# Optimization experiments

Measured on AMD Instinct MI355X. Metric: run time of the kernel, lower is better.

Reference implementation:

```python
import jax, jax.numpy as jnp
import numpy as np

B, T, C = 2, 2048, 1024
N_HEADS = 16
HEAD_DIM = C // N_HEADS

def setup_inputs() -> dict:
    key = jax.random.key(0)
    k1, k2, k3 = jax.random.split(key, 3)
    x = jax.random.normal(k1, (B, T, C), dtype=jnp.float32)
    W_qkv = jax.random.normal(k2, (C, 3 * C), dtype=jnp.float32) * (1.0 / np.sqrt(C))
    W_out = jax.random.normal(k3, (C, C), dtype=jnp.float32) * (1.0 / np.sqrt(C))
    return {"x": x, "W_qkv": W_qkv, "W_out": W_out}

def reference(x, W_qkv, W_out):
    b, t, c = x.shape
    qkv = jnp.einsum('btc,cd->btd', x, W_qkv)  # [B,T,3C]
    q, k, v = jnp.split(qkv, 3, axis=-1)
    # [B, H, T, hd]
    q = q.reshape(b, t, N_HEADS, HEAD_DIM).transpose(0, 2, 1, 3)
    k = k.reshape(b, t, N_HEADS, HEAD_DIM).transpose(0, 2, 1, 3)
    v = v.reshape(b, t, N_HEADS, HEAD_DIM).transpose(0, 2, 1, 3)
    scale = 1.0 / jnp.sqrt(jnp.asarray(HEAD_DIM, dtype=x.dtype))
    attn = jnp.einsum('bhqd,bhkd->bhqk', q, k) * scale  # [B,H,T,T]
    causal = jnp.tril(jnp.ones((t, t), dtype=bool))
    attn = jnp.where(causal, attn, jnp.asarray(-1e9, dtype=attn.dtype))
    attn = jax.nn.softmax(attn, axis=-1)
    out = jnp.einsum('bhqk,bhkd->bhqd', attn, v)
    out = out.transpose(0, 2, 1, 3).reshape(b, t, c)
    return jnp.einsum('btc,cd->btd', out, W_out)
```

## Files before the change

### kernel.cpp

```cpp
#include <hip/hip_runtime.h>
#include <hip/hip_bf16.h>

typedef __attribute__((ext_vector_type(8))) short short8;
typedef __attribute__((ext_vector_type(4))) short bf16x4;
typedef __attribute__((ext_vector_type(4))) float floatx4;

#define T_SEQ 2048
#define NH    16
#define HD    64
#define QSCALE 0.18033688f

#define MFMA16(a, b, c) __builtin_amdgcn_mfma_f32_16x16x16bf16_1k(a, b, c, 0, 0, 0)
#define MFMA32(a, b, c) __builtin_amdgcn_mfma_f32_16x16x32_bf16(a, b, c, 0, 0, 0)

__device__ __forceinline__ ushort f2bf(float f) {
    union { float f; unsigned u; } un; un.f = f;
    unsigned r = un.u + 0x7fff + ((un.u >> 16) & 1);
    return (ushort)(r >> 16);
}
__device__ __forceinline__ unsigned pkbf(float a, float b) {
    __hip_bfloat162 t = __float22bfloat162_rn(float2{a, b});
    return *reinterpret_cast<unsigned*>(&t);
}

typedef const __attribute__((address_space(1))) unsigned int* gp1_t;
typedef __attribute__((address_space(3))) unsigned int* lp3_t;
__device__ __forceinline__ void gl_lds16(const ushort* g, ushort* l) {
    __builtin_amdgcn_global_load_lds((gp1_t)g, (lp3_t)l, 16, 0, 0);
}

__global__ void prep_kernel(const float* __restrict__ Wqkv, const float* __restrict__ Wout,
                            const float* __restrict__ x, ushort* __restrict__ wt_qkv,
                            ushort* __restrict__ wt_out, ushort* __restrict__ x_bf) {
    __shared__ ushort tile[32][33];
    const int bid = blockIdx.x;
    if (bid >= 4096) {
        size_t i = ((size_t)(bid - 4096) * 256 + threadIdx.x) * 8;
        float4 f0 = *(const float4*)(x + i);
        float4 f1 = *(const float4*)(x + i + 4);
        short8 v;
        v[0] = (short)f2bf(f0.x); v[1] = (short)f2bf(f0.y);
        v[2] = (short)f2bf(f0.z); v[3] = (short)f2bf(f0.w);
        v[4] = (short)f2bf(f1.x); v[5] = (short)f2bf(f1.y);
        v[6] = (short)f2bf(f1.z); v[7] = (short)f2bf(f1.w);
        *(short8*)(x_bf + i) = v;
        return;
    }
    const float* in; ushort* out; int R, C, gx, gy;
    if (bid < 3072) { in = Wqkv; out = wt_qkv; R = 1024; C = 3072; gx = bid % 96; gy = bid / 96; }
    else            { int t = bid - 3072; in = Wout; out = wt_out; R = 1024; C = 1024; gx = t & 31; gy = t >> 5; }
    const int tx = threadIdx.x & 31, ty = threadIdx.x >> 5;
    const int bx = gx * 32, by = gy * 32;
    #pragma unroll
    for (int i = ty; i < 32; i += 8)
        tile[i][tx] = f2bf(in[(size_t)(by + i) * C + bx + tx]);
    __syncthreads();
    #pragma unroll
    for (int i = ty; i < 32; i += 8)
        out[(size_t)(bx + i) * R + by + tx] = tile[tx][i];
}

template <int EPI>
__global__ __launch_bounds__(256, 2)
void gemm_bt(const ushort* __restrict__ A, const ushort* __restrict__ Bt,
             void* __restrict__ O0, ushort* __restrict__ O1, ushort* __restrict__ O2,
             int M, int N, int K) {
    __shared__ __align__(16) ushort smem[8704];
    ushort* As = smem;
    ushort* Bs = smem + 4096;
    const int tid  = threadIdx.x;
    const int wave = tid >> 6, lane = tid & 63;
    const int quad = lane >> 4, l16 = lane & 15;
    const int wm = (wave >> 1) * 64, wn = (wave & 1) * 64;
    const int m0 = blockIdx.x * 128, n0 = blockIdx.y * 128;

    const int c0 = tid, c1 = tid + 256;
    const int row0 = c0 >> 2, row1 = c1 >> 2;
    const int g0 = (((c0 & 3) ^ ((row0 >> 1) & 3))) * 8;
    const int g1 = (((c1 & 3) ^ ((row1 >> 1) & 3))) * 8;
    const ushort* aP0 = A  + (size_t)(m0 + row0) * K + g0;
    const ushort* aP1 = A  + (size_t)(m0 + row1) * K + g1;
    const ushort* bP0 = Bt + (size_t)(n0 + row0) * K + g0;
    const ushort* bP1 = Bt + (size_t)(n0 + row1) * K + g1;

    floatx4 acc[4][4];
    #pragma unroll
    for (int i = 0; i < 4; i++)
        #pragma unroll
        for (int j = 0; j < 4; j++)
            acc[i][j] = (floatx4){0.f, 0.f, 0.f, 0.f};

    const int col_sw = (quad ^ ((l16 >> 1) & 3)) * 8;

    for (int k0 = 0; k0 < K; k0 += 32) {
        __syncthreads();
        gl_lds16(aP0 + k0, &As[c0 * 8]);
        gl_lds16(aP1 + k0, &As[c1 * 8]);
        gl_lds16(bP0 + k0, &Bs[c0 * 8]);
        gl_lds16(bP1 + k0, &Bs[c1 * 8]);
        __syncthreads();
        short8 af[4], bf[4];
        #pragma unroll
        for (int i = 0; i < 4; i++)
            af[i] = *(const short8*)(&As[(wm + i * 16 + l16) * 32 + col_sw]);
        #pragma unroll
        for (int j = 0; j < 4; j++)
            bf[j] = *(const short8*)(&Bs[(wn + j * 16 + l16) * 32 + col_sw]);
        #pragma unroll
        for (int i = 0; i < 4; i++)
            #pragma unroll
            for (int j = 0; j < 4; j++)
                acc[i][j] = __builtin_amdgcn_mfma_f32_16x16x32_bf16(af[i], bf[j], acc[i][j], 0, 0, 0);
    }

    if (EPI == 0 && n0 >= 2048) {
        const int b = m0 >> 11;
        const int t0 = m0 & 2047;
        const int head0 = (n0 - 2048) >> 6;
        __syncthreads();
        #pragma unroll
        for (int nh = 0; nh < 2; nh++) {
            if ((wave & 1) == nh) {
                #pragma unroll
                for (int j = 0; j < 4; j++)
                    #pragma unroll
                    for (int i = 0; i < 4; i++) {
                        int nl = j * 16 + l16;
                        int mB = wm + i * 16 + quad * 4;
                        *(unsigned*)(&smem[nl * 136 + mB])     = pkbf(acc[i][j][0], acc[i][j][1]);
                        *(unsigned*)(&smem[nl * 136 + mB + 2]) = pkbf(acc[i][j][2], acc[i][j][3]);
                    }
            }
            __syncthreads();
            #pragma unroll
            for (int cc = 0; cc < 4; cc++) {
                int c = cc * 256 + tid;
                int row = c >> 4, mcol = (c & 15) * 8;
                uint4 v = *(const uint4*)(&smem[row * 136 + mcol]);
                *(uint4*)(&O2[((size_t)(b * NH + head0 + nh) * HD + row) * T_SEQ + t0 + mcol]) = v;
            }
            __syncthreads();
        }
        return;
    }

    #pragma unroll
    for (int i = 0; i < 4; i++) {
        #pragma unroll
        for (int j = 0; j < 4; j++) {
            #pragma unroll
            for (int r = 0; r < 4; r++) {
                int m = m0 + wm + i * 16 + quad * 4 + r;
                int n = n0 + wn + j * 16 + l16;
                if (EPI == 0) {
                    int b = m >> 11, t = m & 2047;
                    int part = n >> 10, c = n & 1023;
                    int head = c >> 6, off = c & 63;
                    float av = acc[i][j][r];
                    if (part == 0) av *= QSCALE;
                    ushort v = f2bf(av);
                    if (part == 0) ((ushort*)O0)[(((size_t)(b * NH + head)) * T_SEQ + t) * HD + off] = v;
                    else           O1[(((size_t)(b * NH + head)) * T_SEQ + t) * HD + off] = v;
                } else {
                    ((float*)O0)[(size_t)m * N + n] = acc[i][j][r];
                }
            }
        }
    }
}

__device__ __forceinline__ void softmax_step(floatx4 s[4], float& mst, float& ll,
                                             floatx4 o[4], bf16x4 pf[4]) {
    float t0 = fmaxf(fmaxf(s[0][0], s[0][1]), fmaxf(s[0][2], s[0][3]));
    float t1 = fmaxf(fmaxf(s[1][0], s[1][1]), fmaxf(s[1][2], s[1][3]));
    float t2 = fmaxf(fmaxf(s[2][0], s[2][1]), fmaxf(s[2][2], s[2][3]));
    float t3 = fmaxf(fmaxf(s[3][0], s[3][1]), fmaxf(s[3][2], s[3][3]));
    float t  = fmaxf(fmaxf(t0, t1), fmaxf(t2, t3));
    if (!__all(t - mst <= 8.0f)) {
        t = fmaxf(t, __shfl_xor(t, 16));
        t = fmaxf(t, __shfl_xor(t, 32));
        float mnew  = fmaxf(mst, t);
        float alpha = exp2f(mst - mnew);
        mst = mnew;
        ll  *= alpha;
        #pragma unroll
        for (int db = 0; db < 4; db++)
            #pragma unroll
            for (int r = 0; r < 4; r++) o[db][r] *= alpha;
    }
    #pragma unroll
    for (int j = 0; j < 4; j++) {
        float p0 = exp2f(s[j][0] - mst);
        float p1 = exp2f(s[j][1] - mst);
        float p2 = exp2f(s[j][2] - mst);
        float p3 = exp2f(s[j][3] - mst);
        ll += (p0 + p1) + (p2 + p3);
        union { bf16x4 v; unsigned u[2]; } pu;
        pu.u[0] = pkbf(p0, p1);
        pu.u[1] = pkbf(p2, p3);
        pf[j] = pu.v;
    }
}

__global__ __launch_bounds__(256, 2)
void attn_kernel(const ushort* __restrict__ Q, const ushort* __restrict__ Kk,
                 const ushort* __restrict__ Vt, ushort* __restrict__ Oout) {
    __shared__ __align__(16) ushort Ks[2][128 * 64];
    __shared__ __align__(16) ushort Vs[2][64 * 128];
    const int tid  = threadIdx.x;
    const int wave = tid >> 6, lane = tid & 63;
    const int quad = lane >> 4, l16 = lane & 15;
    const int idx = blockIdx.x;
    const int bh = idx & 31;
    const int jp = idx >> 5;
    const int p  = (jp < 8) ? jp : (15 - (jp - 8));
    const int qtA = p, qtB = 31 - p;
    const int b = bh >> 4, h = bh & 15;

    const ushort* qp = Q  + (size_t)bh * T_SEQ * HD;
    const ushort* kp = Kk + (size_t)bh * T_SEQ * HD;
    const ushort* vp = Vt + (size_t)bh * HD * T_SEQ;

    const int q0A = qtA * 64 + wave * 16;
    const int q0B = qtB * 64 + wave * 16;

    short8 qfA[2], qfB[2];
    #pragma unroll
    for (int kb = 0; kb < 2; kb++) {
        qfA[kb] = *(const short8*)(qp + (size_t)(q0A + l16) * HD + kb * 32 + quad * 8);
        qfB[kb] = *(const short8*)(qp + (size_t)(q0B + l16) * HD + kb * 32 + quad * 8);
    }

    floatx4 oA[4], oB[4];
    #pragma unroll
    for (int db = 0; db < 4; db++) {
        oA[db] = (floatx4){0.f, 0.f, 0.f, 0.f};
        oB[db] = (floatx4){0.f, 0.f, 0.f, 0.f};
    }
    float mA = -1e30f, llA = 0.f, mB = -1e30f, llB = 0.f;

    int koff[4], voff[4];
    #pragma unroll
    for (int j = 0; j < 4; j++) {
        int c = tid + j * 256;
        int kr = c >> 3;
        koff[j] = kr * HD + (((c & 7) ^ (kr & 7)) * 8);
        int vr = c >> 4;
        voff[j] = vr * T_SEQ + ((((c & 15) ^ (vr & 7))) * 8);
    }

#define STAGE(BUF, I)                                                            \
    {                                                                            \
        const ushort* kg = kp + (size_t)(I) * 128 * HD;                          \
        const ushort* vg = vp + (I) * 128;                                       \
        gl_lds16(kg + koff[0], &Ks[BUF][(tid      ) * 8]);                       \
        gl_lds16(kg + koff[1], &Ks[BUF][(tid + 256) * 8]);                       \
        gl_lds16(kg + koff[2], &Ks[BUF][(tid + 512) * 8]);                       \
        gl_lds16(kg + koff[3], &Ks[BUF][(tid + 768) * 8]);                       \
        gl_lds16(vg + voff[0], &Vs[BUF][(tid      ) * 8]);                       \
        gl_lds16(vg + voff[1], &Vs[BUF][(tid + 256) * 8]);                       \
        gl_lds16(vg + voff[2], &Vs[BUF][(tid + 512) * 8]);                       \
        gl_lds16(vg + voff[3], &Vs[BUF][(tid + 768) * 8]);                       \
    }

    const int xsw = (l16 & 7), qh = quad >> 1, ql = quad & 1;
    const int ka0 = l16 * 64 + ((quad ^ xsw) * 8);
    const int ka1 = l16 * 64 + (((4 + quad) ^ xsw) * 8);
    int va[4];
    #pragma unroll
    for (int jj = 0; jj < 4; jj++)
        va[jj] = l16 * 128 + (((2 * jj + qh) ^ xsw) * 8) + ql * 4;

#define ZS(S) { _Pragma("unroll") for (int z = 0; z < 4; z++) S[z] = (floatx4){0.f, 0.f, 0.f, 0.f}; }

#define QKD(SB, SA, BUF, ST)                                                     \
    {                                                                            \
        _Pragma("unroll")                                                        \
        for (int jj = 0; jj < 4; jj++) {                                         \
            short8 kf = *(const short8*)(&Ks[BUF][(ST) * 4096 + jj * 1024 + ka0]); \
            SB[jj] = MFMA32(kf, qfB[0], SB[jj]);                                 \
            SA[jj] = MFMA32(kf, qfA[0], SA[jj]);                                 \
        }                                                                        \
        _Pragma("unroll")                                                        \
        for (int jj = 0; jj < 4; jj++) {                                         \
            short8 kf = *(const short8*)(&Ks[BUF][(ST) * 4096 + jj * 1024 + ka1]); \
            SB[jj] = MFMA32(kf, qfB[1], SB[jj]);                                 \
            SA[jj] = MFMA32(kf, qfA[1], SA[jj]);                                 \
        }                                                                        \
    }

#define QK1(SB, BUF, ST)                                                         \
    {                                                                            \
        _Pragma("unroll")                                                        \
        for (int jj = 0; jj < 4; jj++) {                                         \
            short8 kf = *(const short8*)(&Ks[BUF][(ST) * 4096 + jj * 1024 + ka0]); \
            SB[jj] = MFMA32(kf, qfB[0], SB[jj]);                                 \
        }                                                                        \
        _Pragma("unroll")                                                        \
        for (int jj = 0; jj < 4; jj++) {                                         \
            short8 kf = *(const short8*)(&Ks[BUF][(ST) * 4096 + jj * 1024 + ka1]); \
            SB[jj] = MFMA32(kf, qfB[1], SB[jj]);                                 \
        }                                                                        \
    }

#define MASKD(S)                                                                 \
    {                                                                            \
        _Pragma("unroll")                                                        \
        for (int jj = 0; jj < 4; jj++)                                           \
            _Pragma("unroll")                                                    \
            for (int rr = 0; rr < 4; rr++)                                       \
                if (jj * 16 + quad * 4 + rr > wave * 16 + l16) S[jj][rr] = -1e30f; \
    }

#define PVG(O, PF, BUF, ST)                                                      \
    {                                                                            \
        _Pragma("unroll")                                                        \
        for (int jj = 0; jj < 4; jj++)                                           \
            _Pragma("unroll")                                                    \
            for (int db = 0; db < 4; db++) {                                     \
                bf16x4 vf = *(const bf16x4*)(&Vs[BUF][va[jj] + (ST) * 64 + db * 2048]); \
                O[db] = MFMA16(vf, PF[jj], O[db]);                               \
            }                                                                    \
    }

#define ITER(BUF, I)                                                             \
    {                                                                            \
        __syncthreads();                                                         \
        if ((I) + 1 < NT) STAGE((BUF) ^ 1, (I) + 1)                              \
        const int kt0 = 2 * (I), kt1 = kt0 + 1;                                  \
        const bool v1 = (kt1 <= qtB);                                            \
        const bool a0 = (kt0 <= qtA), a1 = (kt1 <= qtA);                         \
        floatx4 sB0[4], sB1[4], sA0[4], sA1[4];                                  \
        bf16x4 pfB0[4], pfB1[4], pfA0[4], pfA1[4];                               \
        __builtin_amdgcn_s_setprio(1);                                           \
        ZS(sB0)                                                                  \
        if (a0) { ZS(sA0) QKD(sB0, sA0, BUF, 0) } else { QK1(sB0, BUF, 0) }      \
        if (v1) {                                                                \
            ZS(sB1)                                                              \
            if (a1) { ZS(sA1) QKD(sB1, sA1, BUF, 1) } else { QK1(sB1, BUF, 1) }  \
        }                                                                        \
        __builtin_amdgcn_s_setprio(0);                                           \
        if (kt0 == qtB) { MASKD(sB0) }                                           \
        if (v1 && kt1 == qtB) { MASKD(sB1) }                                     \
        if (a0 && kt0 == qtA) { MASKD(sA0) }                                     \
        if (a1 && kt1 == qtA) { MASKD(sA1) }                                     \
        softmax_step(sB0, mB, llB, oB, pfB0);                                    \
        PVG(oB, pfB0, BUF, 0)                                                    \
        if (v1) { softmax_step(sB1, mB, llB, oB, pfB1); PVG(oB, pfB1, BUF, 1) }  \
        if (a0) { softmax_step(sA0, mA, llA, oA, pfA0); PVG(oA, pfA0, BUF, 0) }  \
        if (a1) { softmax_step(sA1, mA, llA, oA, pfA1); PVG(oA, pfA1, BUF, 1) }  \
    }

    const int NT = (qtB + 2) >> 1;
    STAGE(0, 0)

    int i = 0;
    for (; i + 1 < NT; i += 2) {
        ITER(0, i)
        ITER(1, i + 1)
    }
    if (i < NT) ITER(0, i)
#undef ITER
#undef PVG
#undef MASKD
#undef QK1
#undef QKD
#undef ZS
#undef STAGE

    {
        float lB = llB;
        lB += __shfl_xor(lB, 16);
        lB += __shfl_xor(lB, 32);
        const float inv = 1.0f / lB;
        const int t = q0B + l16;
        #pragma unroll
        for (int db = 0; db < 4; db++) {
            union { ushort4 w; unsigned u[2]; } ou;
            ou.u[0] = pkbf(oB[db][0] * inv, oB[db][1] * inv);
            ou.u[1] = pkbf(oB[db][2] * inv, oB[db][3] * inv);
            *(ushort4*)(Oout + (((size_t)b * T_SEQ + t) * NH + h) * HD + db * 16 + quad * 4) = ou.w;
        }
    }
    {
        float lA = llA;
        lA += __shfl_xor(lA, 16);
        lA += __shfl_xor(lA, 32);
        const float inv = 1.0f / lA;
        const int t = q0A + l16;
        #pragma unroll
        for (int db = 0; db < 4; db++) {
            union { ushort4 w; unsigned u[2]; } ou;
            ou.u[0] = pkbf(oA[db][0] * inv, oA[db][1] * inv);
            ou.u[1] = pkbf(oA[db][2] * inv, oA[db][3] * inv);
            *(ushort4*)(Oout + (((size_t)b * T_SEQ + t) * NH + h) * HD + db * 16 + quad * 4) = ou.w;
        }
    }
}

extern "C" void kernel_launch(void* const* d_in, const int* in_sizes, int n_in,
                              void* d_out, int out_size, void* d_ws, size_t ws_size,
                              hipStream_t stream) {
    const float* x    = (const float*)d_in[0];
    const float* Wqkv = (const float*)d_in[1];
    const float* Wout = (const float*)d_in[2];
    ushort* ws = (ushort*)d_ws;

    ushort* wt_qkv = ws;
    ushort* wt_out = wt_qkv + 3072 * 1024;
    ushort* q_ws   = wt_out + 1024 * 1024;
    ushort* k_ws   = q_ws + 4194304;
    ushort* v_t    = k_ws + 4194304;
    ushort* a_out  = v_t + 4194304;
    ushort* x_bf   = a_out + 4194304;

    prep_kernel<<<dim3(6144), 256, 0, stream>>>(Wqkv, Wout, x, wt_qkv, wt_out, x_bf);

    gemm_bt<0><<<dim3(32, 24), 256, 0, stream>>>(x_bf, wt_qkv, q_ws, k_ws, v_t, 4096, 3072, 1024);

    attn_kernel<<<dim3(512), 256, 0, stream>>>(q_ws, k_ws, v_t, a_out);

    gemm_bt<1><<<dim3(32, 8), 256, 0, stream>>>(a_out, wt_out, (float*)d_out, nullptr, nullptr,
                                                4096, 1024, 1024);
}
```

Before: 179.7 us.

## Accumulate softmax row sums via MFMA, zero-C QK MFMAs, and swizzle GEMM tiles

```diff
diff --git a/kernel.cpp b/kernel.cpp
--- a/kernel.cpp
+++ b/kernel.cpp
@@ -72,7 +72,13 @@
     const int wave = tid >> 6, lane = tid & 63;
     const int quad = lane >> 4, l16 = lane & 15;
     const int wm = (wave >> 1) * 64, wn = (wave & 1) * 64;
-    const int m0 = blockIdx.x * 128, n0 = blockIdx.y * 128;
+
+    const int nwg = gridDim.x * gridDim.y;
+    const int lid = blockIdx.y * gridDim.x + blockIdx.x;
+    const int cpx = nwg >> 3;
+    const int swz = (lid & 7) * cpx + (lid >> 3);
+    const int m0 = (swz / gridDim.y) * 128;
+    const int n0 = (swz % gridDim.y) * 128;
 
     const int c0 = tid, c1 = tid + 256;
     const int row0 = c0 >> 2, row1 = c1 >> 2;
@@ -169,7 +175,7 @@
     }
 }
 
-__device__ __forceinline__ void softmax_step(floatx4 s[4], float& mst, float& ll,
+__device__ __forceinline__ void softmax_step(floatx4 s[4], float& mst, floatx4& ll4,
                                              floatx4 o[4], bf16x4 pf[4]) {
     float t0 = fmaxf(fmaxf(s[0][0], s[0][1]), fmaxf(s[0][2], s[0][3]));
     float t1 = fmaxf(fmaxf(s[1][0], s[1][1]), fmaxf(s[1][2], s[1][3]));
@@ -182,7 +188,7 @@
         float mnew  = fmaxf(mst, t);
         float alpha = exp2f(mst - mnew);
         mst = mnew;
-        ll  *= alpha;
+        ll4 *= alpha;
         #pragma unroll
         for (int db = 0; db < 4; db++)
             #pragma unroll
@@ -194,7 +200,6 @@
         float p1 = exp2f(s[j][1] - mst);
         float p2 = exp2f(s[j][2] - mst);
         float p3 = exp2f(s[j][3] - mst);
-        ll += (p0 + p1) + (p2 + p3);
         union { bf16x4 v; unsigned u[2]; } pu;
         pu.u[0] = pkbf(p0, p1);
         pu.u[1] = pkbf(p2, p3);
@@ -231,13 +236,14 @@
         qfB[kb] = *(const short8*)(qp + (size_t)(q0B + l16) * HD + kb * 32 + quad * 8);
     }
 
+    const floatx4 FZ4 = (floatx4){0.f, 0.f, 0.f, 0.f};
+    const bf16x4 vfone = {(short)0x3F80, (short)0x3F80, (short)0x3F80, (short)0x3F80};
+
     floatx4 oA[4], oB[4];
     #pragma unroll
-    for (int db = 0; db < 4; db++) {
-        oA[db] = (floatx4){0.f, 0.f, 0.f, 0.f};
-        oB[db] = (floatx4){0.f, 0.f, 0.f, 0.f};
-    }
-    float mA = -1e30f, llA = 0.f, mB = -1e30f, llB = 0.f;
+    for (int db = 0; db < 4; db++) { oA[db] = FZ4; oB[db] = FZ4; }
+    floatx4 lA4 = FZ4, lB4 = FZ4;
+    float mA = -1e30f, mB = -1e30f;
 
     int koff[4], voff[4];
     #pragma unroll
@@ -271,15 +277,13 @@
     for (int jj = 0; jj < 4; jj++)
         va[jj] = l16 * 128 + (((2 * jj + qh) ^ xsw) * 8) + ql * 4;
 
-#define ZS(S) { _Pragma("unroll") for (int z = 0; z < 4; z++) S[z] = (floatx4){0.f, 0.f, 0.f, 0.f}; }
-
-#define QKD(SB, SA, BUF, ST)                                                     \
+#define QKD2(SB, SA, BUF, ST)                                                    \
     {                                                                            \
         _Pragma("unroll")                                                        \
         for (int jj = 0; jj < 4; jj++) {                                         \
             short8 kf = *(const short8*)(&Ks[BUF][(ST) * 4096 + jj * 1024 + ka0]); \
-            SB[jj] = MFMA32(kf, qfB[0], SB[jj]);                                 \
-            SA[jj] = MFMA32(kf, qfA[0], SA[jj]);                                 \
+            SB[jj] = MFMA32(kf, qfB[0], FZ4);                                    \
+            SA[jj] = MFMA32(kf, qfA[0], FZ4);                                    \
         }                                                                        \
         _Pragma("unroll")                                                        \
         for (int jj = 0; jj < 4; jj++) {                                         \
@@ -289,12 +293,12 @@
         }                                                                        \
     }
 
-#define QK1(SB, BUF, ST)                                                         \
+#define QK12(SB, BUF, ST)                                                        \
     {                                                                            \
         _Pragma("unroll")                                                        \
         for (int jj = 0; jj < 4; jj++) {                                         \
             short8 kf = *(const short8*)(&Ks[BUF][(ST) * 4096 + jj * 1024 + ka0]); \
-            SB[jj] = MFMA32(kf, qfB[0], SB[jj]);                                 \
+            SB[jj] = MFMA32(kf, qfB[0], FZ4);                                    \
         }                                                                        \
         _Pragma("unroll")                                                        \
         for (int jj = 0; jj < 4; jj++) {                                         \
@@ -321,6 +325,12 @@
                 bf16x4 vf = *(const bf16x4*)(&Vs[BUF][va[jj] + (ST) * 64 + db * 2048]); \
                 O[db] = MFMA16(vf, PF[jj], O[db]);                               \
             }                                                                    \
+    }
+
+#define LACC(L4, PF)                                                             \
+    {                                                                            \
+        _Pragma("unroll")                                                        \
+        for (int jj = 0; jj < 4; jj++) L4 = MFMA16(vfone, PF[jj], L4);           \
     }
 
 #define ITER(BUF, I)                                                             \
@@ -333,22 +343,18 @@
         floatx4 sB0[4], sB1[4], sA0[4], sA1[4];                                  \
         bf16x4 pfB0[4], pfB1[4], pfA0[4], pfA1[4];                               \
         __builtin_amdgcn_s_setprio(1);                                           \
-        ZS(sB0)                                                                  \
-        if (a0) { ZS(sA0) QKD(sB0, sA0, BUF, 0) } else { QK1(sB0, BUF, 0) }      \
-        if (v1) {                                                                \
-            ZS(sB1)                                                              \
-            if (a1) { ZS(sA1) QKD(sB1, sA1, BUF, 1) } else { QK1(sB1, BUF, 1) }  \
-        }                                                                        \
+        if (a0) { QKD2(sB0, sA0, BUF, 0) } else { QK12(sB0, BUF, 0) }            \
+        if (v1) { if (a1) { QKD2(sB1, sA1, BUF, 1) } else { QK12(sB1, BUF, 1) } }\
         __builtin_amdgcn_s_setprio(0);                                           \
         if (kt0 == qtB) { MASKD(sB0) }                                           \
         if (v1 && kt1 == qtB) { MASKD(sB1) }                                     \
         if (a0 && kt0 == qtA) { MASKD(sA0) }                                     \
         if (a1 && kt1 == qtA) { MASKD(sA1) }                                     \
-        softmax_step(sB0, mB, llB, oB, pfB0);                                    \
-        PVG(oB, pfB0, BUF, 0)                                                    \
-        if (v1) { softmax_step(sB1, mB, llB, oB, pfB1); PVG(oB, pfB1, BUF, 1) }  \
-        if (a0) { softmax_step(sA0, mA, llA, oA, pfA0); PVG(oA, pfA0, BUF, 0) }  \
-        if (a1) { softmax_step(sA1, mA, llA, oA, pfA1); PVG(oA, pfA1, BUF, 1) }  \
+        softmax_step(sB0, mB, lB4, oB, pfB0);                                    \
+        PVG(oB, pfB0, BUF, 0) LACC(lB4, pfB0)                                    \
+        if (v1) { softmax_step(sB1, mB, lB4, oB, pfB1); PVG(oB, pfB1, BUF, 1) LACC(lB4, pfB1) } \
+        if (a0) { softmax_step(sA0, mA, lA4, oA, pfA0); PVG(oA, pfA0, BUF, 0) LACC(lA4, pfA0) } \
+        if (a1) { softmax_step(sA1, mA, lA4, oA, pfA1); PVG(oA, pfA1, BUF, 1) LACC(lA4, pfA1) } \
     }
 
     const int NT = (qtB + 2) >> 1;
@@ -361,18 +367,15 @@
     }
     if (i < NT) ITER(0, i)
 #undef ITER
+#undef LACC
 #undef PVG
 #undef MASKD
-#undef QK1
-#undef QKD
-#undef ZS
+#undef QK12
+#undef QKD2
 #undef STAGE
 
     {
-        float lB = llB;
-        lB += __shfl_xor(lB, 16);
-        lB += __shfl_xor(lB, 32);
-        const float inv = 1.0f / lB;
+        const float inv = 1.0f / lB4[0];
         const int t = q0B + l16;
         #pragma unroll
         for (int db = 0; db < 4; db++) {
@@ -383,10 +386,7 @@
         }
     }
     {
-        float lA = llA;
-        lA += __shfl_xor(lA, 16);
-        lA += __shfl_xor(lA, 32);
-        const float inv = 1.0f / lA;
+        const float inv = 1.0f / lA4[0];
         const int t = q0A + l16;
         #pragma unroll
         for (int db = 0; db < 4; db++) {
```

New measurement: 181.7 us. No clear change (+1.1%).

## Double GEMM K-tile to 64 with new LDS swizzle and XCD-aware block remap

Applied to the files above, without the earlier changes.

```diff
diff --git a/kernel.cpp b/kernel.cpp
--- a/kernel.cpp
+++ b/kernel.cpp
@@ -65,23 +65,31 @@
 void gemm_bt(const ushort* __restrict__ A, const ushort* __restrict__ Bt,
              void* __restrict__ O0, ushort* __restrict__ O1, ushort* __restrict__ O2,
              int M, int N, int K) {
-    __shared__ __align__(16) ushort smem[8704];
+    __shared__ __align__(16) ushort smem[16384];
     ushort* As = smem;
-    ushort* Bs = smem + 4096;
+    ushort* Bs = smem + 8192;
     const int tid  = threadIdx.x;
     const int wave = tid >> 6, lane = tid & 63;
     const int quad = lane >> 4, l16 = lane & 15;
     const int wm = (wave >> 1) * 64, wn = (wave & 1) * 64;
-    const int m0 = blockIdx.x * 128, n0 = blockIdx.y * 128;
-
-    const int c0 = tid, c1 = tid + 256;
-    const int row0 = c0 >> 2, row1 = c1 >> 2;
-    const int g0 = (((c0 & 3) ^ ((row0 >> 1) & 3))) * 8;
-    const int g1 = (((c1 & 3) ^ ((row1 >> 1) & 3))) * 8;
-    const ushort* aP0 = A  + (size_t)(m0 + row0) * K + g0;
-    const ushort* aP1 = A  + (size_t)(m0 + row1) * K + g1;
-    const ushort* bP0 = Bt + (size_t)(n0 + row0) * K + g0;
-    const ushort* bP1 = Bt + (size_t)(n0 + row1) * K + g1;
+
+    const int nwg = gridDim.x * gridDim.y;
+    const int lid = blockIdx.y * gridDim.x + blockIdx.x;
+    const int cpx = nwg >> 3;
+    const int swz = (lid & 7) * cpx + (lid >> 3);
+    const int m0 = (swz / gridDim.y) * 128;
+    const int n0 = (swz % gridDim.y) * 128;
+
+    const ushort* aP[4];
+    const ushort* bP[4];
+    #pragma unroll
+    for (int j = 0; j < 4; j++) {
+        int c = tid + j * 256;
+        int r = c >> 3;
+        int g = ((c & 7) ^ (r & 7)) * 8;
+        aP[j] = A  + (size_t)(m0 + r) * K + g;
+        bP[j] = Bt + (size_t)(n0 + r) * K + g;
+    }
 
     floatx4 acc[4][4];
     #pragma unroll
@@ -90,27 +98,30 @@
         for (int j = 0; j < 4; j++)
             acc[i][j] = (floatx4){0.f, 0.f, 0.f, 0.f};
 
-    const int col_sw = (quad ^ ((l16 >> 1) & 3)) * 8;
-
-    for (int k0 = 0; k0 < K; k0 += 32) {
+    const int xsw = l16 & 7;
+
+    for (int k0 = 0; k0 < K; k0 += 64) {
         __syncthreads();
-        gl_lds16(aP0 + k0, &As[c0 * 8]);
-        gl_lds16(aP1 + k0, &As[c1 * 8]);
-        gl_lds16(bP0 + k0, &Bs[c0 * 8]);
-        gl_lds16(bP1 + k0, &Bs[c1 * 8]);
+        #pragma unroll
+        for (int j = 0; j < 4; j++) gl_lds16(aP[j] + k0, &As[(tid + j * 256) * 8]);
+        #pragma unroll
+        for (int j = 0; j < 4; j++) gl_lds16(bP[j] + k0, &Bs[(tid + j * 256) * 8]);
         __syncthreads();
-        short8 af[4], bf[4];
-        #pragma unroll
-        for (int i = 0; i < 4; i++)
-            af[i] = *(const short8*)(&As[(wm + i * 16 + l16) * 32 + col_sw]);
-        #pragma unroll
-        for (int j = 0; j < 4; j++)
-            bf[j] = *(const short8*)(&Bs[(wn + j * 16 + l16) * 32 + col_sw]);
-        #pragma unroll
-        for (int i = 0; i < 4; i++)
+        #pragma unroll
+        for (int kk = 0; kk < 2; kk++) {
+            short8 af[4], bf[4];
+            #pragma unroll
+            for (int i = 0; i < 4; i++)
+                af[i] = *(const short8*)(&As[(wm + i * 16 + l16) * 64 + ((kk * 4 + quad) ^ xsw) * 8]);
             #pragma unroll
             for (int j = 0; j < 4; j++)
-                acc[i][j] = __builtin_amdgcn_mfma_f32_16x16x32_bf16(af[i], bf[j], acc[i][j], 0, 0, 0);
+                bf[j] = *(const short8*)(&Bs[(wn + j * 16 + l16) * 64 + ((kk * 4 + quad) ^ xsw) * 8]);
+            #pragma unroll
+            for (int i = 0; i < 4; i++)
+                #pragma unroll
+                for (int j = 0; j < 4; j++)
+                    acc[i][j] = MFMA32(af[i], bf[j], acc[i][j]);
+        }
     }
 
     if (EPI == 0 && n0 >= 2048) {
```

Result: no change. 176.9 us (-1.6%).
